# Kernel optimization log

Hardware: AMD Instinct MI355X
Metric: run time of the kernel (lower is better)

## Reference

```python
import jax, jax.numpy as jnp
import numpy as np

B, L = 512, 24576
HID = 10


def setup_inputs() -> dict:
    key = jax.random.key(0)
    ks = jax.random.split(key, 9)
    s = 0.1
    return {
        "x": jax.random.normal(ks[0], (B, L, 1), dtype=jnp.float32),
        "conv_w": jax.random.normal(ks[1], (1, 1, 3), dtype=jnp.float32) * s,
        "conv_b": jax.random.normal(ks[2], (1,), dtype=jnp.float32) * s,
        "w_ih": jax.random.normal(ks[3], (4 * HID, 1), dtype=jnp.float32) * s,
        "w_hh": jax.random.normal(ks[4], (4 * HID, HID), dtype=jnp.float32) * s,
        "b_ih": jax.random.normal(ks[5], (4 * HID,), dtype=jnp.float32) * s,
        "b_hh": jax.random.normal(ks[6], (4 * HID,), dtype=jnp.float32) * s,
        "mlp_w": jax.random.normal(ks[7], (3, HID), dtype=jnp.float32) * s,
        "mlp_b": jax.random.normal(ks[8], (3,), dtype=jnp.float32) * s,
    }


def reference(x, conv_w, conv_b, w_ih, w_hh, b_ih, b_hh, mlp_w, mlp_b):
    b, l, _ = x.shape
    lp = l // 3  # conv1d k=3 stride=3 -> non-overlapping windows
    seg = x[:, : lp * 3, 0].reshape(b, lp, 3)
    c = jnp.einsum('blk,k->bl', seg, conv_w[0, 0]) + conv_b[0]
    c = jax.nn.relu(c)  # (B, Lp)
    seq = c.T[:, :, None]  # (Lp, B, 1) seq-major, input_size=1
    # precompute input-side gate pre-activations for all timesteps
    xg = jnp.einsum('tbi,gi->tbg', seq, w_ih) + b_ih + b_hh  # (Lp, B, 4H)

    def step(carry, xg_t):
        h, cc = carry
        g = xg_t + h @ w_hh.T  # (B, 4H)
        i, f, gg, o = jnp.split(g, 4, axis=-1)  # torch gate order i,f,g,o
        i = jax.nn.sigmoid(i)
        f = jax.nn.sigmoid(f)
        gg = jnp.tanh(gg)
        o = jax.nn.sigmoid(o)
        cc = f * cc + i * gg
        h = o * jnp.tanh(cc)
        return (h, cc), None

    h0 = jnp.zeros((b, HID), dtype=x.dtype)
    (h_n, _), _ = jax.lax.scan(step, (h0, h0), xg)
    return h_n @ mlp_w.T + mlp_b  # (B, 3)
```

## Files before the change

### kernel.cpp

```cpp
#include <hip/hip_runtime.h>


#define DEV __device__ __forceinline__

DEV float rl_f(float v, int lane) {
  return __int_as_float(__builtin_amdgcn_readlane(__float_as_int(v), lane));
}

template <int CTRL>
DEV float quad_bcast(float v) {
#if __has_builtin(__builtin_amdgcn_mov_dpp)
  return __int_as_float(__builtin_amdgcn_mov_dpp(__float_as_int(v), CTRL, 0xF, 0xF, true));
#else
  return __int_as_float(__builtin_amdgcn_update_dpp(0, __float_as_int(v), CTRL, 0xF, 0xF, true));
#endif
}

DEV float fast_exp2(float x) {
#if __has_builtin(__builtin_amdgcn_exp2f)
  return __builtin_amdgcn_exp2f(x);
#else
  return __exp2f(x);
#endif
}

DEV float fast_rcp(float x) { return __builtin_amdgcn_rcpf(x); }

constexpr int kB = 512;
constexpr int kL = 24576;
constexpr int kLp = 8192;
constexpr int kHid = 10;
constexpr int kChunk = 64;
constexpr int kNChunk = kLp / kChunk;

__global__ __launch_bounds__(256, 1) void lstm_fused(
    const float* __restrict__ x,
    const float* __restrict__ conv_w,
    const float* __restrict__ conv_b,
    const float* __restrict__ w_ih,
    const float* __restrict__ w_hh,
    const float* __restrict__ b_ih,
    const float* __restrict__ b_hh,
    const float* __restrict__ mlp_w,
    const float* __restrict__ mlp_b,
    float* __restrict__ out) {
  const int lane = threadIdx.x & 63;
  const int wave = threadIdx.x >> 6;
  const int b = blockIdx.x * 4 + wave;

  const int hid = lane >> 2;
  const int gt = lane & 3;
  const bool active = (lane < 40);
  const int r = active ? (gt * kHid + hid) : 0;

  const float cw0 = conv_w[0], cw1 = conv_w[1], cw2 = conv_w[2];
  const float cbv = conv_b[0];

  const float wih = w_ih[r];
  const float bsum = b_ih[r] + b_hh[r];
  const float* wr = w_hh + r * kHid;
  const float w0 = wr[0], w1 = wr[1], w2 = wr[2], w3 = wr[3], w4 = wr[4];
  const float w5 = wr[5], w6 = wr[6], w7 = wr[7], w8 = wr[8], w9 = wr[9];

  constexpr float kL2E = 1.4426950408889634f;
  const float smul = (gt == 2) ? (-2.0f * kL2E) : (-kL2E);

  const float* xb = x + (size_t)b * kL;
  const int xoff = lane * 3;

  float x0 = xb[xoff + 0];
  float x1 = xb[xoff + 1];
  float x2 = xb[xoff + 2];

  float h = 0.0f;
  float cst = 0.0f;

  for (int ch = 0; ch < kNChunk; ++ch) {
    float ct = fmaf(x2, cw2, fmaf(x1, cw1, fmaf(x0, cw0, cbv)));
    ct = fmaxf(ct, 0.0f);

    if (ch + 1 < kNChunk) {
      const float* xn = xb + (size_t)(ch + 1) * (kChunk * 3) + xoff;
      x0 = xn[0];
      x1 = xn[1];
      x2 = xn[2];
    }

#pragma unroll 8
    for (int t = 0; t < kChunk; ++t) {
      const float ctv = rl_f(ct, t);
      const float xg = fmaf(ctv, wih, bsum);

      float p0 = fmaf(rl_f(h, 0), w0, xg);
      p0 = fmaf(rl_f(h, 4), w1, p0);
      p0 = fmaf(rl_f(h, 8), w2, p0);
      p0 = fmaf(rl_f(h, 12), w3, p0);
      p0 = fmaf(rl_f(h, 16), w4, p0);
      float p1 = rl_f(h, 20) * w5;
      p1 = fmaf(rl_f(h, 24), w6, p1);
      p1 = fmaf(rl_f(h, 28), w7, p1);
      p1 = fmaf(rl_f(h, 32), w8, p1);
      p1 = fmaf(rl_f(h, 36), w9, p1);
      const float pre = p0 + p1;

      const float a = fast_rcp(1.0f + fast_exp2(pre * smul));

      const float iv = quad_bcast<0x00>(a);
      const float fv = quad_bcast<0x55>(a);
      const float gv = quad_bcast<0xAA>(a);
      const float ov = quad_bcast<0xFF>(a);

      const float u = fmaf(iv * gv, 2.0f, -iv);
      cst = fmaf(fv, cst, u);

      const float s2 = fast_rcp(1.0f + fast_exp2(cst * (-2.0f * kL2E)));
      h = fmaf(ov * s2, 2.0f, -ov);
    }
  }

  if (lane < 3) {
    const float* mw = mlp_w + lane * kHid;
    float acc = mlp_b[lane];
    acc = fmaf(rl_f(h, 0), mw[0], acc);
    acc = fmaf(rl_f(h, 4), mw[1], acc);
    acc = fmaf(rl_f(h, 8), mw[2], acc);
    acc = fmaf(rl_f(h, 12), mw[3], acc);
    acc = fmaf(rl_f(h, 16), mw[4], acc);
    acc = fmaf(rl_f(h, 20), mw[5], acc);
    acc = fmaf(rl_f(h, 24), mw[6], acc);
    acc = fmaf(rl_f(h, 28), mw[7], acc);
    acc = fmaf(rl_f(h, 32), mw[8], acc);
    acc = fmaf(rl_f(h, 36), mw[9], acc);
    out[b * 3 + lane] = acc;
  }
}

extern "C" void kernel_launch(void* const* d_in, const int* in_sizes, int n_in,
                              void* d_out, int out_size, void* d_ws, size_t ws_size,
                              hipStream_t stream) {
  const float* x = (const float*)d_in[0];
  const float* conv_w = (const float*)d_in[1];
  const float* conv_b = (const float*)d_in[2];
  const float* w_ih = (const float*)d_in[3];
  const float* w_hh = (const float*)d_in[4];
  const float* b_ih = (const float*)d_in[5];
  const float* b_hh = (const float*)d_in[6];
  const float* mlp_w = (const float*)d_in[7];
  const float* mlp_b = (const float*)d_in[8];
  float* out = (float*)d_out;

  dim3 grid(kB / 4), block(256);
  hipLaunchKernelGGL(lstm_fused, grid, block, 0, stream, x, conv_w, conv_b,
                     w_ih, w_hh, b_ih, b_hh, mlp_w, mlp_b, out);
}
```

Baseline: 815.9 us.

## Fold gate scaling into weights, tree the recurrent dot, one wave per block

Pre-scales the input, recurrent and bias weights by the per-gate exp2 factor, and keeps the cell state in a pre-scaled domain. This removes multiplies from the serial per-timestep dependency chain. The 10-term recurrent dot product is split into four partial sums instead of two, shortening the FMA chain. The launch changes from 128 blocks of 4 waves to 512 single-wave blocks, so waves spread across more CUs. Rounding order changes slightly because of the rescaling and reassociation.

```diff
diff --git a/kernel.cpp b/kernel.cpp
--- a/kernel.cpp
+++ b/kernel.cpp
@@ -33,7 +33,7 @@
 constexpr int kChunk = 64;
 constexpr int kNChunk = kLp / kChunk;
 
-__global__ __launch_bounds__(256, 1) void lstm_fused(
+__global__ __launch_bounds__(64, 1) void lstm_fused(
     const float* __restrict__ x,
     const float* __restrict__ conv_w,
     const float* __restrict__ conv_b,
@@ -45,8 +45,7 @@
     const float* __restrict__ mlp_b,
     float* __restrict__ out) {
   const int lane = threadIdx.x & 63;
-  const int wave = threadIdx.x >> 6;
-  const int b = blockIdx.x * 4 + wave;
+  const int b = blockIdx.x;
 
   const int hid = lane >> 2;
   const int gt = lane & 3;
@@ -56,14 +55,19 @@
   const float cw0 = conv_w[0], cw1 = conv_w[1], cw2 = conv_w[2];
   const float cbv = conv_b[0];
 
-  const float wih = w_ih[r];
-  const float bsum = b_ih[r] + b_hh[r];
-  const float* wr = w_hh + r * kHid;
-  const float w0 = wr[0], w1 = wr[1], w2 = wr[2], w3 = wr[3], w4 = wr[4];
-  const float w5 = wr[5], w6 = wr[6], w7 = wr[7], w8 = wr[8], w9 = wr[9];
-
   constexpr float kL2E = 1.4426950408889634f;
   const float smul = (gt == 2) ? (-2.0f * kL2E) : (-kL2E);
+
+  const float wih = w_ih[r] * smul;
+  const float bsum = (b_ih[r] + b_hh[r]) * smul;
+  const float* wr = w_hh + r * kHid;
+  const float w0 = wr[0] * smul, w1 = wr[1] * smul, w2 = wr[2] * smul;
+  const float w3 = wr[3] * smul, w4 = wr[4] * smul, w5 = wr[5] * smul;
+  const float w6 = wr[6] * smul, w7 = wr[7] * smul, w8 = wr[8] * smul;
+  const float w9 = wr[9] * smul;
+
+  const float C4 = -4.0f * kL2E;
+  const float C2 = 2.0f * kL2E;
 
   const float* xb = x + (size_t)b * kL;
   const int xoff = lane * 3;
@@ -73,7 +77,7 @@
   float x2 = xb[xoff + 2];
 
   float h = 0.0f;
-  float cst = 0.0f;
+  float cs = 0.0f;
 
   for (int ch = 0; ch < kNChunk; ++ch) {
     float ct = fmaf(x2, cw2, fmaf(x1, cw1, fmaf(x0, cw0, cbv)));
@@ -91,30 +95,37 @@
       const float ctv = rl_f(ct, t);
       const float xg = fmaf(ctv, wih, bsum);
 
-      float p0 = fmaf(rl_f(h, 0), w0, xg);
-      p0 = fmaf(rl_f(h, 4), w1, p0);
-      p0 = fmaf(rl_f(h, 8), w2, p0);
-      p0 = fmaf(rl_f(h, 12), w3, p0);
-      p0 = fmaf(rl_f(h, 16), w4, p0);
-      float p1 = rl_f(h, 20) * w5;
-      p1 = fmaf(rl_f(h, 24), w6, p1);
-      p1 = fmaf(rl_f(h, 28), w7, p1);
-      p1 = fmaf(rl_f(h, 32), w8, p1);
-      p1 = fmaf(rl_f(h, 36), w9, p1);
-      const float pre = p0 + p1;
+      const float h0 = rl_f(h, 0), h1 = rl_f(h, 4), h2 = rl_f(h, 8);
+      const float h3 = rl_f(h, 12), h4 = rl_f(h, 16), h5 = rl_f(h, 20);
+      const float h6 = rl_f(h, 24), h7 = rl_f(h, 28), h8 = rl_f(h, 32);
+      const float h9 = rl_f(h, 36);
+      float pA = fmaf(h0, w0, xg);
+      pA = fmaf(h1, w1, pA);
+      pA = fmaf(h2, w2, pA);
+      float pB = h3 * w3;
+      pB = fmaf(h4, w4, pB);
+      pB = fmaf(h5, w5, pB);
+      float pC = h6 * w6;
+      pC = fmaf(h7, w7, pC);
+      float pD = h8 * w8;
+      pD = fmaf(h9, w9, pD);
+      const float pre = (pA + pB) + (pC + pD);
 
-      const float a = fast_rcp(1.0f + fast_exp2(pre * smul));
+      const float a = fast_rcp(1.0f + fast_exp2(pre));
 
       const float iv = quad_bcast<0x00>(a);
       const float fv = quad_bcast<0x55>(a);
       const float gv = quad_bcast<0xAA>(a);
       const float ov = quad_bcast<0xFF>(a);
+      const float ov2 = ov + ov;
 
-      const float u = fmaf(iv * gv, 2.0f, -iv);
-      cst = fmaf(fv, cst, u);
+      const float pig = iv * gv;
+      const float ti = iv * C2;
+      const float u2 = fmaf(pig, C4, ti);
+      cs = fmaf(fv, cs, u2);
 
-      const float s2 = fast_rcp(1.0f + fast_exp2(cst * (-2.0f * kL2E)));
-      h = fmaf(ov * s2, 2.0f, -ov);
+      const float s2 = fast_rcp(1.0f + fast_exp2(cs));
+      h = fmaf(s2, ov2, -ov);
     }
   }
 
@@ -149,7 +160,7 @@
   const float* mlp_b = (const float*)d_in[8];
   float* out = (float*)d_out;
 
-  dim3 grid(kB / 4), block(256);
+  dim3 grid(kB), block(64);
   hipLaunchKernelGGL(lstm_fused, grid, block, 0, stream, x, conv_w, conv_b,
                      w_ih, w_hh, b_ih, b_hh, mlp_w, mlp_b, out);
 }
```

Result: no change. 817.7 us (+0.2%).
